# Performance work log

Hardware: AMD Instinct MI355X
Metric: run time of the kernel (lower is better)

Reference implementation:

```python
import jax, jax.numpy as jnp
import numpy as np

STRIDES = [8, 16, 32, 64, 128]
HW = [(100, 128), (50, 64), (25, 32), (13, 16), (7, 8)]
SCORE_THR = 0.05
IOU_THR = 0.6
MAX_DET = 1000
MAX_OUT = 100  # fixed pad size in _post_process


def _coords(h, w, stride):
    # FCOS coords_fmap2orig: center of each cell in original image coords
    sx = jnp.arange(w, dtype=jnp.float32) * stride + stride // 2
    sy = jnp.arange(h, dtype=jnp.float32) * stride + stride // 2
    yy, xx = jnp.meshgrid(sy, sx, indexing='ij')
    return jnp.stack([xx.reshape(-1), yy.reshape(-1)], axis=-1)  # [h*w, 2]


def _reshape_cat(feats):
    # list of [B,C,h,w] -> [B, sum(h*w), C]
    outs = [f.transpose(0, 2, 3, 1).reshape(f.shape[0], -1, f.shape[1]) for f in feats]
    return jnp.concatenate(outs, axis=1)


def _nms_single(scores, classes, boxes):
    # scores [N] (sorted desc), classes [N] int, boxes [N,4]; greedy DIoU-NMS
    N = scores.shape[0]
    valid = scores >= SCORE_THR
    # batched_nms: offset boxes by class so cross-class boxes never overlap
    max_coord = jnp.max(jnp.where(valid[:, None], boxes, -jnp.inf))
    offs = classes.astype(boxes.dtype) * (max_coord + 1.0)
    b = boxes + offs[:, None]
    x1, y1, x2, y2 = b[:, 0], b[:, 1], b[:, 2], b[:, 3]
    areas = (x2 - x1 + 1.0) * (y2 - y1 + 1.0)
    cx, cy = (x1 + x2) * 0.5, (y1 + y2) * 0.5
    xmin = jnp.maximum(x1[:, None], x1[None, :]); ymin = jnp.maximum(y1[:, None], y1[None, :])
    xmax = jnp.minimum(x2[:, None], x2[None, :]); ymax = jnp.minimum(y2[:, None], y2[None, :])
    inter = jnp.clip(xmax - xmin, 0) * jnp.clip(ymax - ymin, 0)
    iou = inter / (areas[:, None] + areas[None, :] - inter)
    inter_diag = (cx[:, None] - cx[None, :]) ** 2 + (cy[:, None] - cy[None, :]) ** 2
    oxmin = jnp.minimum(x1[:, None], x1[None, :]); oymin = jnp.minimum(y1[:, None], y1[None, :])
    oxmax = jnp.maximum(x2[:, None], x2[None, :]); oymax = jnp.maximum(y2[:, None], y2[None, :])
    outer_diag = (oxmax - oxmin) ** 2 + (oymax - oymin) ** 2
    diou = iou - inter_diag / jnp.maximum(outer_diag, 1e-12)
    idxs = jnp.arange(N)

    def body(i, keep):
        sup = keep[i] & (idxs > i) & (diou[i] > IOU_THR)
        return keep & (~sup)

    keep = jax.lax.fori_loop(0, N, body, valid)
    # kept boxes in descending-score order, padded with -2 to MAX_OUT
    rank = jnp.cumsum(keep) - 1
    pos = jnp.where(keep, jnp.minimum(rank, MAX_OUT), MAX_OUT)  # slot MAX_OUT is dumped
    out_s = jnp.full((MAX_OUT + 1,), -2.0, scores.dtype).at[pos].set(jnp.where(keep, scores, -2.0))[:MAX_OUT]
    out_c = jnp.full((MAX_OUT + 1,), -2, classes.dtype).at[pos].set(jnp.where(keep, classes, -2))[:MAX_OUT]
    out_b = jnp.full((MAX_OUT + 1, 4), -2.0, boxes.dtype).at[pos].set(jnp.where(keep[:, None], boxes, -2.0))[:MAX_OUT]
    return out_s, out_c, out_b


def _forward(cls_feats, reg_feats):
    cls_logits = _reshape_cat(cls_feats)          # [B, L, C]
    reg_preds = _reshape_cat(reg_feats)           # [B, L, 4]
    coords = jnp.concatenate([_coords(h, w, s) for (h, w), s in zip(HW, STRIDES)], axis=0)
    cls_preds = jax.nn.sigmoid(cls_logits)
    cls_scores = jnp.max(cls_preds, axis=-1)      # [B, L]
    cls_classes = jnp.argmax(cls_preds, axis=-1) + 1
    x1y1 = coords[None] - reg_preds[..., :2]
    x2y2 = coords[None] + reg_preds[..., 2:]
    boxes = jnp.concatenate([x1y1, x2y2], axis=-1)  # [B, L, 4]
    max_num = min(MAX_DET, cls_scores.shape[-1])
    topv, topi = jax.lax.top_k(cls_scores, max_num)  # sorted descending
    top_c = jnp.take_along_axis(cls_classes, topi, axis=1)
    top_b = jnp.take_along_axis(boxes, topi[..., None], axis=1)
    return jax.vmap(_nms_single)(topv, top_c, top_b)


def setup_inputs() -> dict:
    key = jax.random.key(0)
    ks = jax.random.split(key, 16)
    inp = {}
    C = 80
    for i, (h, w) in enumerate(HW):
        inp[f'cls{i}'] = jax.random.normal(ks[i], (16, C, h, w), dtype=jnp.float32)
        # ltrb offsets scaled so boxes are realistically sized and overlap
        inp[f'reg{i}'] = jax.random.uniform(ks[5 + i], (16, 4, h, w), dtype=jnp.float32) * 64.0
    inp['boxes_anchor'] = jax.random.normal(ks[10], (16, 100, 4), dtype=jnp.float32)
    inp['labels_anchor'] = jax.random.randint(ks[11], (16, 100), 0, 80)
    inp['score_anchor'] = jax.random.uniform(ks[12], (16, 100), dtype=jnp.float32)
    return inp


def reference(cls0, cls1, cls2, cls3, cls4, reg0, reg1, reg2, reg3, reg4,
              boxes_anchor, labels_anchor, score_anchor):
    # nms_anchor (boxes_anchor, labels_anchor, score_anchor) is consumed but
    # does not affect the output in the original forward.
    scores, classes, boxes = _forward([cls0, cls1, cls2, cls3, cls4],
                                      [reg0, reg1, reg2, reg3, reg4])
    return scores, classes, boxes
```

## Files before the change

kernel.cpp:

```cpp
#include <hip/hip_runtime.h>
#include <math.h>

typedef unsigned int u32;
typedef unsigned long long u64;

#define BB 16
#define NANCH 17064
#define NGRP 4266
#define NTOP 1000
#define NWORD 16
#define NOUT 100
#define NBIN13 8192
#define NSPLIT 17

__device__ __forceinline__ u32 fmap(float v) {
    u32 u = __float_as_uint(v);
    return (u & 0x80000000u) ? ~u : (u | 0x80000000u);
}
__device__ __forceinline__ float funmap(u32 u) {
    u32 b = (u & 0x80000000u) ? (u & 0x7FFFFFFFu) : ~u;
    return __uint_as_float(b);
}

__global__ void __launch_bounds__(256) k_anchor(
        const float* __restrict__ c0, const float* __restrict__ c1,
        const float* __restrict__ c2, const float* __restrict__ c3,
        const float* __restrict__ c4,
        const float* __restrict__ r0, const float* __restrict__ r1,
        const float* __restrict__ r2, const float* __restrict__ r3,
        const float* __restrict__ r4,
        u32* __restrict__ akey, int* __restrict__ aclass,
        float* __restrict__ abox, u32* __restrict__ ghist) {
    __shared__ u32 h1[NBIN13];
    int tid = threadIdx.x;
    int b = blockIdx.y;
    int gt = blockIdx.x * 256 + tid;
    bool valid = gt < 4 * NGRP;

    for (int i = tid; i < NBIN13; i += 256) h1[i] = 0;
    __syncthreads();

    if (valid) {
        int p = gt >> 2, cs = gt & 3;
        int a = p * 4;

        const float *cp, *rp;
        int loc, wl, h, stride, half;
        if (a < 12800)      { loc = a;         wl = 7; h = 100; stride = 8;   half = 4;  cp = c0; rp = r0; }
        else if (a < 16000) { loc = a - 12800; wl = 6; h = 50;  stride = 16;  half = 8;  cp = c1; rp = r1; }
        else if (a < 16800) { loc = a - 16000; wl = 5; h = 25;  stride = 32;  half = 16; cp = c2; rp = r2; }
        else if (a < 17008) { loc = a - 16800; wl = 4; h = 13;  stride = 64;  half = 32; cp = c3; rp = r3; }
        else                { loc = a - 17008; wl = 3; h = 7;   stride = 128; half = 64; cp = c4; rp = r4; }
        int y = loc >> wl, x = loc & ((1 << wl) - 1);
        int hw = h << wl, hwq = hw >> 2;

        const float4* cb4 = (const float4*)(cp + (size_t)b * 80 * hw +
                                            (size_t)cs * 20 * hw + loc);
        float4 buf[20];
#pragma unroll
        for (int c = 0; c < 20; ++c) buf[c] = cb4[(size_t)c * hwq];
        const float4* rb4 = (const float4*)(rp + (size_t)b * 4 * hw + loc);
        float4 gl, gt_, gr, gb;
        if (cs == 0) {
            gl = rb4[0]; gt_ = rb4[hwq]; gr = rb4[2 * hwq]; gb = rb4[3 * hwq];
        }
        __builtin_amdgcn_sched_barrier(0);

        int cbase = cs * 20;
        float m0 = buf[0].x, m1 = buf[0].y, m2 = buf[0].z, m3 = buf[0].w;
        int a0 = cbase, a1 = cbase, a2 = cbase, a3 = cbase;
#pragma unroll
        for (int c = 1; c < 20; ++c) {
            float4 u = buf[c];
            int cc = cbase + c;
            if (u.x > m0) { m0 = u.x; a0 = cc; }
            if (u.y > m1) { m1 = u.y; a1 = cc; }
            if (u.z > m2) { m2 = u.z; a2 = cc; }
            if (u.w > m3) { m3 = u.w; a3 = cc; }
        }
        {
            bool low = (cs & 1) == 0;
            float pm; int pa; bool tk;
            pm = __shfl_xor(m0, 1); pa = __shfl_xor(a0, 1);
            tk = low ? (m0 >= pm) : (m0 > pm); m0 = tk ? m0 : pm; a0 = tk ? a0 : pa;
            pm = __shfl_xor(m1, 1); pa = __shfl_xor(a1, 1);
            tk = low ? (m1 >= pm) : (m1 > pm); m1 = tk ? m1 : pm; a1 = tk ? a1 : pa;
            pm = __shfl_xor(m2, 1); pa = __shfl_xor(a2, 1);
            tk = low ? (m2 >= pm) : (m2 > pm); m2 = tk ? m2 : pm; a2 = tk ? a2 : pa;
            pm = __shfl_xor(m3, 1); pa = __shfl_xor(a3, 1);
            tk = low ? (m3 >= pm) : (m3 > pm); m3 = tk ? m3 : pm; a3 = tk ? a3 : pa;
        }
        {
            bool low = (cs & 2) == 0;
            float pm; int pa; bool tk;
            pm = __shfl_xor(m0, 2); pa = __shfl_xor(a0, 2);
            tk = low ? (m0 >= pm) : (m0 > pm); m0 = tk ? m0 : pm; a0 = tk ? a0 : pa;
            pm = __shfl_xor(m1, 2); pa = __shfl_xor(a1, 2);
            tk = low ? (m1 >= pm) : (m1 > pm); m1 = tk ? m1 : pm; a1 = tk ? a1 : pa;
            pm = __shfl_xor(m2, 2); pa = __shfl_xor(a2, 2);
            tk = low ? (m2 >= pm) : (m2 > pm); m2 = tk ? m2 : pm; a2 = tk ? a2 : pa;
            pm = __shfl_xor(m3, 2); pa = __shfl_xor(a3, 2);
            tk = low ? (m3 >= pm) : (m3 > pm); m3 = tk ? m3 : pm; a3 = tk ? a3 : pa;
        }
        if (cs == 0) {
            int idx = b * NANCH + a;
            u32 km0 = fmap(m0), km1 = fmap(m1), km2 = fmap(m2), km3 = fmap(m3);
            *(uint4*)(akey + idx) = make_uint4(km0, km1, km2, km3);
            *(int4*)(aclass + idx) = make_int4(a0 + 1, a1 + 1, a2 + 1, a3 + 1);
            atomicAdd(&h1[km0 >> 19], 1u);
            atomicAdd(&h1[km1 >> 19], 1u);
            atomicAdd(&h1[km2 >> 19], 1u);
            atomicAdd(&h1[km3 >> 19], 1u);
            float cy = (float)(y * stride + half);
            float cx0 = (float)(x * stride + half);
            float gls[4] = {gl.x, gl.y, gl.z, gl.w};
            float gts[4] = {gt_.x, gt_.y, gt_.z, gt_.w};
            float grs[4] = {gr.x, gr.y, gr.z, gr.w};
            float gbs[4] = {gb.x, gb.y, gb.z, gb.w};
#pragma unroll
            for (int k = 0; k < 4; ++k) {
                float cx = cx0 + (float)(k * stride);
                *(float4*)(abox + (size_t)(idx + k) * 4) =
                    make_float4(cx - gls[k], cy - gts[k], cx + grs[k], cy + gbs[k]);
            }
        }
    }
    __syncthreads();
    u32* gh = ghist + (size_t)b * NBIN13;
    for (int i = tid; i < NBIN13; i += 256) {
        u32 c = h1[i];
        if (c) atomicAdd(&gh[i], c);
    }
}

__global__ void __launch_bounds__(256) k_thresh(
        const u32* __restrict__ akey, const u32* __restrict__ ghist,
        u32* __restrict__ thr) {
    __shared__ u32 h1[NBIN13];
    __shared__ u32 seg[256];
    __shared__ u32 binb[32];
    __shared__ int Gs;
    __shared__ u32 T13s, As;
    int b = blockIdx.x, t = threadIdx.x;
    const uint4* ak4 = (const uint4*)(akey + (size_t)b * NANCH);

    {
        const uint4* g4 = (const uint4*)(ghist + (size_t)b * NBIN13);
        uint4* h4 = (uint4*)h1;
        for (int i = t; i < NBIN13 / 4; i += 256) h4[i] = g4[i];
    }
    if (t == 0) Gs = 0;
    __syncthreads();
    u32 s = 0;
#pragma unroll
    for (int j = 0; j < 32; ++j) s += h1[t * 32 + ((j + t) & 31)];
    seg[t] = s;
    __syncthreads();
    for (int off = 1; off < 256; off <<= 1) {
        u32 v = seg[t];
        u32 add = (t + off < 256) ? seg[t + off] : 0u;
        __syncthreads();
        seg[t] = v + add;
        __syncthreads();
    }
    if (seg[t] >= NTOP) atomicMax(&Gs, t);
    __syncthreads();
    int G = Gs;
    u32 hi = (G < 255) ? seg[G + 1] : 0u;
    if (t < 32) binb[t] = h1[G * 32 + t];
    __syncthreads();
    if (t == 0) {
        u32 acc = hi, A = hi;
        int T13 = G * 32;
        for (int i = 31; i >= 0; --i) {
            A = acc;
            acc += binb[i];
            if (acc >= NTOP) { T13 = G * 32 + i; break; }
        }
        T13s = (u32)T13; As = A;
        Gs = 0;
    }
    __syncthreads();
    u32 T13 = T13s, A = As;
    for (int i = t; i < NBIN13; i += 256) h1[i] = 0;
    __syncthreads();
    for (int i = t; i < NANCH / 4; i += 256) {
        uint4 k4 = ak4[i];
        if ((k4.x >> 19) == T13) atomicAdd(&h1[(k4.x >> 6) & (NBIN13 - 1)], 1u);
        if ((k4.y >> 19) == T13) atomicAdd(&h1[(k4.y >> 6) & (NBIN13 - 1)], 1u);
        if ((k4.z >> 19) == T13) atomicAdd(&h1[(k4.z >> 6) & (NBIN13 - 1)], 1u);
        if ((k4.w >> 19) == T13) atomicAdd(&h1[(k4.w >> 6) & (NBIN13 - 1)], 1u);
    }
    __syncthreads();
    u32 target = NTOP - A;
    u32 s2 = 0;
#pragma unroll
    for (int j = 0; j < 32; ++j) s2 += h1[t * 32 + ((j + t) & 31)];
    seg[t] = s2;
    __syncthreads();
    for (int off = 1; off < 256; off <<= 1) {
        u32 v = seg[t];
        u32 add = (t + off < 256) ? seg[t + off] : 0u;
        __syncthreads();
        seg[t] = v + add;
        __syncthreads();
    }
    if (seg[t] >= target) atomicMax(&Gs, t);
    __syncthreads();
    int G2 = Gs;
    u32 hi2 = (G2 < 255) ? seg[G2 + 1] : 0u;
    if (t == 0) {
        u32 acc = hi2;
        int t2 = G2 * 32;
        for (int i = 31; i >= 0; --i) {
            acc += h1[G2 * 32 + i];
            if (acc >= target) { t2 = G2 * 32 + i; break; }
        }
        thr[b] = (T13 << 13) | (u32)t2;
    }
}

__global__ void __launch_bounds__(256) k_compact(const u32* __restrict__ akey,
                                                 const u32* __restrict__ thr,
                                                 u32* __restrict__ ccnt,
                                                 u64* __restrict__ cand) {
    __shared__ u32 lcnt, baseoff;
    int b = blockIdx.y, s = blockIdx.x, t = threadIdx.x;
    if (t == 0) lcnt = 0;
    __syncthreads();
    u32 T = thr[b];

    int base = s * 1024;
    int n = min(1024, NANCH - base);
    u32 kk[4]; u32 pos[4]; bool m[4] = {false, false, false, false};
    if (4 * t < n) {
        uint4 k4 = *(const uint4*)(akey + (size_t)b * NANCH + base + 4 * t);
        kk[0] = k4.x; kk[1] = k4.y; kk[2] = k4.z; kk[3] = k4.w;
#pragma unroll
        for (int i = 0; i < 4; ++i) {
            m[i] = (kk[i] >> 6) >= T;
            if (m[i]) pos[i] = atomicAdd(&lcnt, 1u);
        }
    }
    __syncthreads();
    if (t == 0) baseoff = atomicAdd(&ccnt[b], lcnt);
    __syncthreads();
    u32 bo = baseoff;
    u64* cb = cand + (size_t)b * NANCH;
#pragma unroll
    for (int i = 0; i < 4; ++i) {
        if (m[i])
            cb[bo + pos[i]] =
                ((u64)kk[i] << 32) | (u64)(0xFFFFFFFFu - (u32)(base + 4 * t + i));
    }
}

__global__ void __launch_bounds__(256) k_rank(
        const u64* __restrict__ cand, const u32* __restrict__ ccnt,
        const int* __restrict__ aclass, const float* __restrict__ abox,
        float* __restrict__ tscore, int* __restrict__ tclass,
        float* __restrict__ tbox, u32* __restrict__ maxcU) {
    __shared__ u64 tile[2048];
    int b = blockIdx.y, tid = threadIdx.x;
    int C = (int)ccnt[b];
    const u64* ck = cand + (size_t)b * NANCH;
    for (int base = blockIdx.x * 256; base < C; base += gridDim.x * 256) {
        int i = base + tid;
        bool have = i < C;
        u64 my = have ? ck[i] : 0ull;
        int rank = 0;
        for (int t0 = 0; t0 < C; t0 += 2048) {
            int nt = min(2048, C - t0);
            __syncthreads();
            for (int j = tid; j < nt; j += 256) tile[j] = ck[t0 + j];
            __syncthreads();
            int q0 = 0, q1 = 0, q2 = 0, q3 = 0, q4 = 0, q5 = 0, q6 = 0, q7 = 0;
            int j = 0;
            for (; j + 8 <= nt; j += 8) {
                u64 v0 = tile[j + 0], v1 = tile[j + 1];
                u64 v2 = tile[j + 2], v3 = tile[j + 3];
                u64 v4 = tile[j + 4], v5 = tile[j + 5];
                u64 v6 = tile[j + 6], v7 = tile[j + 7];
                q0 += v0 > my; q1 += v1 > my; q2 += v2 > my; q3 += v3 > my;
                q4 += v4 > my; q5 += v5 > my; q6 += v6 > my; q7 += v7 > my;
            }
            for (; j < nt; ++j) q0 += tile[j] > my;
            rank += ((q0 + q1) + (q2 + q3)) + ((q4 + q5) + (q6 + q7));
        }
        u32 mymax = 0;
        if (have && rank < NTOP) {
            u32 a = 0xFFFFFFFFu - (u32)(my & 0xFFFFFFFFull);
            int src = b * NANCH + (int)a;
            int dst = b * NTOP + rank;
            float logit = funmap((u32)(my >> 32));
            float sc = 1.0f / (1.0f + expf(-logit));
            float b0 = abox[src * 4 + 0], b1 = abox[src * 4 + 1];
            float b2 = abox[src * 4 + 2], b3 = abox[src * 4 + 3];
            tscore[dst] = sc;
            tclass[dst] = aclass[src];
            tbox[dst * 4 + 0] = b0;
            tbox[dst * 4 + 1] = b1;
            tbox[dst * 4 + 2] = b2;
            tbox[dst * 4 + 3] = b3;
            if (sc >= 0.05f)
                mymax = fmap(fmaxf(fmaxf(b0, b1), fmaxf(b2, b3)));
        }
        for (int off = 32; off > 0; off >>= 1) {
            u32 o = (u32)__shfl_down((int)mymax, off);
            mymax = mymax > o ? mymax : o;
        }
        if ((tid & 63) == 0) atomicMax(&maxcU[b], mymax);
    }
}

__global__ void k_sup(const float* __restrict__ tbox, const int* __restrict__ tclass,
                      const u32* __restrict__ maxcU, u64* __restrict__ sup) {
    int u = blockIdx.x, b = blockIdx.y;
    int ti = 0, rem = u;
    while (rem >= NWORD - ti) { rem -= NWORD - ti; ++ti; }
    int tj = ti + rem;
    int t = threadIdx.x;
    __shared__ double jx1[64], jy1[64], jx2[64], jy2[64], jcx[64], jcy[64], jar[64];
    double mc1 = (double)funmap(maxcU[b]) + 1.0;
    int j = tj * 64 + t;
    if (j < NTOP) {
        const float* bx = tbox + (size_t)(b * NTOP + j) * 4;
        double o = (double)tclass[b * NTOP + j] * mc1;
        double x1 = (double)bx[0] + o, y1 = (double)bx[1] + o;
        double x2 = (double)bx[2] + o, y2 = (double)bx[3] + o;
        jx1[t] = x1; jy1[t] = y1; jx2[t] = x2; jy2[t] = y2;
        jcx[t] = (x1 + x2) * 0.5; jcy[t] = (y1 + y2) * 0.5;
        jar[t] = (x2 - x1 + 1.0) * (y2 - y1 + 1.0);
    }
    __syncthreads();
    int i = ti * 64 + t;
    if (i >= NTOP) return;
    const float* bx = tbox + (size_t)(b * NTOP + i) * 4;
    double o = (double)tclass[b * NTOP + i] * mc1;
    double ix1 = (double)bx[0] + o, iy1 = (double)bx[1] + o;
    double ix2 = (double)bx[2] + o, iy2 = (double)bx[3] + o;
    double icx = (ix1 + ix2) * 0.5, icy = (iy1 + iy2) * 0.5;
    double iar = (ix2 - ix1 + 1.0) * (iy2 - iy1 + 1.0);
    u64 bits = 0;
    int jbase = tj * 64;
    for (int jj = 0; jj < 64; ++jj) {
        int jg = jbase + jj;
        if (jg >= NTOP) break;
        if (jg <= i) continue;
        double xm = fmax(ix1, jx1[jj]), ym = fmax(iy1, jy1[jj]);
        double xM = fmin(ix2, jx2[jj]), yM = fmin(iy2, jy2[jj]);
        double inter = fmax(xM - xm, 0.0) * fmax(yM - ym, 0.0);
        double U = iar + jar[jj] - inter;
        double dx = icx - jcx[jj], dy = icy - jcy[jj];
        double idg = dx * dx + dy * dy;
        double ox = fmax(ix2, jx2[jj]) - fmin(ix1, jx1[jj]);
        double oy = fmax(iy2, jy2[jj]) - fmin(iy1, jy1[jj]);
        double odg = fmax(ox * ox + oy * oy, 1e-12);
        if (inter * odg - idg * U > 0.6 * (U * odg)) bits |= (1ull << jj);
    }
    sup[(size_t)(b * NTOP + i) * NWORD + tj] = bits;
}

__global__ void __launch_bounds__(256) k_scan(
        const u64* __restrict__ sup, const float* __restrict__ tscore,
        const int* __restrict__ tclass, const float* __restrict__ tbox,
        float* __restrict__ out) {
    int b = blockIdx.x, tid = threadIdx.x;
    int lane = tid & 63;
    __shared__ u64 tl[2][64 * 17];
    __shared__ float sc_s[1024];
    __shared__ int kept_lds[NOUT];
    __shared__ int kept_sh;
    const u64* supb = sup + (size_t)b * NTOP * NWORD;
    for (int i = tid; i < 1024; i += 256)
        sc_s[i] = (i < NTOP) ? tscore[b * NTOP + i] : -1.0f;
    if (tid == 0) kept_sh = 0;
    for (int q = 0; q < 4; ++q) {
        int e = q * 256 + tid;
        int rr = e >> 4, w = e & 15;
        tl[0][rr * 17 + w] = (rr < NTOP) ? supb[(size_t)rr * 16 + w] : 0ull;
    }
    __syncthreads();
    u64 remw = 0;
    int kept = 0;
    for (int t = 0; t < NWORD; ++t) {
        int cur = t & 1;
        if (tid >= 64) {
            if (t + 1 < NWORD) {
                int r1 = (t + 1) * 64;
                for (int e = tid - 64; e < 1024; e += 192) {
                    int rr = r1 + (e >> 4), w = e & 15;
                    tl[cur ^ 1][(e >> 4) * 17 + w] =
                        (rr < NTOP) ? supb[(size_t)rr * 16 + w] : 0ull;
                }
            }
        } else {
            int r0 = t * 64;
            int r = r0 + lane;
            float s = sc_s[r];
            u64 vmask = __ballot(s >= 0.05f);
            u64 M = tl[cur][lane * 17 + t];
            u64 rem_t = __shfl(remw, t);
            u64 cnd = vmask & ~rem_t;
            u64 keepmask = 0;
            while (cnd) {
                int k = __ffsll(cnd) - 1;
                keepmask |= 1ull << k;
                if (lane == 0) kept_lds[kept] = r0 + k;
                ++kept;
                if (kept >= NOUT) break;
                u64 Mk = __shfl(M, k);
                cnd &= ~(Mk | (1ull << k));
            }
            if (lane < NWORD) {
                u64 km = keepmask;
                while (km) {
                    int k = __ffsll(km) - 1;
                    km &= km - 1;
                    remw |= tl[cur][k * 17 + lane];
                }
            }
            if (lane == 0) kept_sh = kept;
        }
        __syncthreads();
        if (kept_sh >= NOUT) break;
    }
    float* os = out + b * NOUT;
    float* oc = out + BB * NOUT + b * NOUT;
    float* ob = out + 2 * BB * NOUT + (size_t)b * NOUT * 4;
    for (int i = tid; i < NOUT; i += 256) { os[i] = -2.0f; oc[i] = -2.0f; }
    for (int i = tid; i < NOUT * 4; i += 256) ob[i] = -2.0f;
    __syncthreads();
    int ncopy = kept_sh < NOUT ? kept_sh : NOUT;
    for (int r = tid; r < ncopy; r += 256) {
        int i = kept_lds[r];
        os[r] = tscore[b * NTOP + i];
        oc[r] = (float)tclass[b * NTOP + i];
        ob[r * 4 + 0] = tbox[(size_t)(b * NTOP + i) * 4 + 0];
        ob[r * 4 + 1] = tbox[(size_t)(b * NTOP + i) * 4 + 1];
        ob[r * 4 + 2] = tbox[(size_t)(b * NTOP + i) * 4 + 2];
        ob[r * 4 + 3] = tbox[(size_t)(b * NTOP + i) * 4 + 3];
    }
}

extern "C" void kernel_launch(void* const* d_in, const int* in_sizes, int n_in,
                              void* d_out, int out_size, void* d_ws, size_t ws_size,
                              hipStream_t stream) {
    (void)in_sizes; (void)n_in; (void)out_size; (void)ws_size;
    const float* cls[5];
    const float* reg[5];
    for (int i = 0; i < 5; ++i) {
        cls[i] = (const float*)d_in[2 * i];
        reg[i] = (const float*)d_in[2 * i + 1];
    }
    float* out = (float*)d_out;

    char* ws = (char*)d_ws;
    u32* ghist = (u32*)ws;           ws += (size_t)BB * NBIN13 * sizeof(u32);
    u32* ccnt = (u32*)ws;            ws += 64;
    u32* maxcU = (u32*)ws;           ws += 64;
    size_t zbytes = (size_t)BB * NBIN13 * sizeof(u32) + 128;
    u32* thr = (u32*)ws;             ws += 64;
    u64* cand = (u64*)ws;            ws += (size_t)BB * NANCH * sizeof(u64);
    u64* sup = (u64*)ws;             ws += (size_t)BB * NTOP * NWORD * sizeof(u64);
    u32* akey = (u32*)ws;            ws += (size_t)BB * NANCH * sizeof(u32);
    int* aclass = (int*)ws;          ws += (size_t)BB * NANCH * sizeof(int);
    float* abox = (float*)ws;        ws += (size_t)BB * NANCH * 4 * sizeof(float);
    float* tscore = (float*)ws;      ws += (size_t)BB * NTOP * sizeof(float);
    int* tclass = (int*)ws;          ws += (size_t)BB * NTOP * sizeof(int);
    float* tbox = (float*)ws;        ws += (size_t)BB * NTOP * 4 * sizeof(float);

    hipMemsetAsync(ghist, 0, zbytes, stream);

    k_anchor<<<dim3((4 * NGRP + 255) / 256, BB), 256, 0, stream>>>(
        cls[0], cls[1], cls[2], cls[3], cls[4],
        reg[0], reg[1], reg[2], reg[3], reg[4],
        akey, aclass, abox, ghist);
    k_thresh<<<BB, 256, 0, stream>>>(akey, ghist, thr);
    k_compact<<<dim3(NSPLIT, BB), 256, 0, stream>>>(akey, thr, ccnt, cand);
    k_rank<<<dim3(5, BB), 256, 0, stream>>>(cand, ccnt, aclass, abox,
                                            tscore, tclass, tbox, maxcU);
    k_sup<<<dim3(136, BB), 64, 0, stream>>>(tbox, tclass, maxcU, sup);
    k_scan<<<BB, 256, 0, stream>>>(sup, tscore, tclass, tbox, out);
}
```

Baseline: 226.6 us.

## Use coarse 13-bit histogram threshold only; enlarge rank grid for extra candidates

Drops the second refinement pass in the threshold kernel, which re-scanned all anchor keys to build a fine histogram inside the boundary bin. Compaction now keeps every anchor whose top 13 key bits reach the coarse bin, so more than 1000 candidates pass to ranking. The rank kernel grid grows from 5 to 14 blocks per image to cover the larger candidate set. This removes a full key pass plus scans, but adds ranking work and depends on the rank kernel handling variable candidate counts correctly.

```diff
diff --git a/kernel.cpp b/kernel.cpp
--- a/kernel.cpp
+++ b/kernel.cpp
@@ -134,15 +134,12 @@
 }
 
 __global__ void __launch_bounds__(256) k_thresh(
-        const u32* __restrict__ akey, const u32* __restrict__ ghist,
-        u32* __restrict__ thr) {
+        const u32* __restrict__ ghist, u32* __restrict__ thr) {
     __shared__ u32 h1[NBIN13];
     __shared__ u32 seg[256];
     __shared__ u32 binb[32];
     __shared__ int Gs;
-    __shared__ u32 T13s, As;
     int b = blockIdx.x, t = threadIdx.x;
-    const uint4* ak4 = (const uint4*)(akey + (size_t)b * NANCH);
 
     {
         const uint4* g4 = (const uint4*)(ghist + (size_t)b * NBIN13);
@@ -170,53 +167,13 @@
     if (t < 32) binb[t] = h1[G * 32 + t];
     __syncthreads();
     if (t == 0) {
-        u32 acc = hi, A = hi;
+        u32 acc = hi;
         int T13 = G * 32;
         for (int i = 31; i >= 0; --i) {
-            A = acc;
             acc += binb[i];
             if (acc >= NTOP) { T13 = G * 32 + i; break; }
         }
-        T13s = (u32)T13; As = A;
-        Gs = 0;
-    }
-    __syncthreads();
-    u32 T13 = T13s, A = As;
-    for (int i = t; i < NBIN13; i += 256) h1[i] = 0;
-    __syncthreads();
-    for (int i = t; i < NANCH / 4; i += 256) {
-        uint4 k4 = ak4[i];
-        if ((k4.x >> 19) == T13) atomicAdd(&h1[(k4.x >> 6) & (NBIN13 - 1)], 1u);
-        if ((k4.y >> 19) == T13) atomicAdd(&h1[(k4.y >> 6) & (NBIN13 - 1)], 1u);
-        if ((k4.z >> 19) == T13) atomicAdd(&h1[(k4.z >> 6) & (NBIN13 - 1)], 1u);
-        if ((k4.w >> 19) == T13) atomicAdd(&h1[(k4.w >> 6) & (NBIN13 - 1)], 1u);
-    }
-    __syncthreads();
-    u32 target = NTOP - A;
-    u32 s2 = 0;
-#pragma unroll
-    for (int j = 0; j < 32; ++j) s2 += h1[t * 32 + ((j + t) & 31)];
-    seg[t] = s2;
-    __syncthreads();
-    for (int off = 1; off < 256; off <<= 1) {
-        u32 v = seg[t];
-        u32 add = (t + off < 256) ? seg[t + off] : 0u;
-        __syncthreads();
-        seg[t] = v + add;
-        __syncthreads();
-    }
-    if (seg[t] >= target) atomicMax(&Gs, t);
-    __syncthreads();
-    int G2 = Gs;
-    u32 hi2 = (G2 < 255) ? seg[G2 + 1] : 0u;
-    if (t == 0) {
-        u32 acc = hi2;
-        int t2 = G2 * 32;
-        for (int i = 31; i >= 0; --i) {
-            acc += h1[G2 * 32 + i];
-            if (acc >= target) { t2 = G2 * 32 + i; break; }
-        }
-        thr[b] = (T13 << 13) | (u32)t2;
+        thr[b] = (u32)T13;
     }
 }
 
@@ -238,7 +195,7 @@
         kk[0] = k4.x; kk[1] = k4.y; kk[2] = k4.z; kk[3] = k4.w;
 #pragma unroll
         for (int i = 0; i < 4; ++i) {
-            m[i] = (kk[i] >> 6) >= T;
+            m[i] = (kk[i] >> 19) >= T;
             if (m[i]) pos[i] = atomicAdd(&lcnt, 1u);
         }
     }
@@ -476,10 +433,10 @@
         cls[0], cls[1], cls[2], cls[3], cls[4],
         reg[0], reg[1], reg[2], reg[3], reg[4],
         akey, aclass, abox, ghist);
-    k_thresh<<<BB, 256, 0, stream>>>(akey, ghist, thr);
+    k_thresh<<<BB, 256, 0, stream>>>(ghist, thr);
     k_compact<<<dim3(NSPLIT, BB), 256, 0, stream>>>(akey, thr, ccnt, cand);
-    k_rank<<<dim3(5, BB), 256, 0, stream>>>(cand, ccnt, aclass, abox,
-                                            tscore, tclass, tbox, maxcU);
+    k_rank<<<dim3(14, BB), 256, 0, stream>>>(cand, ccnt, aclass, abox,
+                                             tscore, tclass, tbox, maxcU);
     k_sup<<<dim3(136, BB), 64, 0, stream>>>(tbox, tclass, maxcU, sup);
     k_scan<<<BB, 256, 0, stream>>>(sup, tscore, tclass, tbox, out);
 }
```

Measured after the change: 219.8 us. 1.03x faster.
